# Kernel tuning notes

Hardware: AMD Instinct MI355X
Metric: run time of the kernel (lower is better)

Reference implementation:

```python
import jax, jax.numpy as jnp
import numpy as np

# Genotype (DARTS RNN): 8 recurrent steps (activation, predecessor index) + concat indices
GENO = [("relu", 0), ("relu", 1), ("tanh", 2), ("relu", 3),
        ("relu", 4), ("identity", 1), ("relu", 5), ("relu", 1)]
CONCAT = [1, 2, 3, 4, 5, 6, 7, 8]
NINP, NHID = 256, 256
T, B = 1024, 64
INITRANGE = 0.04

_ACT = {"tanh": jnp.tanh, "relu": jax.nn.relu,
        "sigmoid": jax.nn.sigmoid, "identity": lambda v: v}


def setup_inputs() -> dict:
    key = jax.random.key(0)
    k1, k2, k3, k4 = jax.random.split(key, 4)
    inputs = jax.random.normal(k1, (T, B, NINP), dtype=jnp.float32)
    hidden = jax.random.normal(k2, (1, B, NHID), dtype=jnp.float32)
    W0 = jax.random.uniform(k3, (NINP + NHID, 2 * NHID), dtype=jnp.float32,
                            minval=-INITRANGE, maxval=INITRANGE)
    Ws = jax.random.uniform(k4, (len(GENO), NHID, 2 * NHID), dtype=jnp.float32,
                            minval=-INITRANGE, maxval=INITRANGE)
    return {"inputs": inputs, "hidden": hidden, "W0": W0, "Ws": Ws}


def _cell(x, h_prev, W0, Ws):
    # init state: s0 = h_prev + sigmoid(c0) * (tanh(h0) - h_prev)
    xh = jnp.concatenate([x, h_prev], axis=-1)          # [B, ninp+nhid]
    c0, h0 = jnp.split(xh @ W0, 2, axis=-1)             # each [B, nhid]
    s0 = h_prev + jax.nn.sigmoid(c0) * (jnp.tanh(h0) - h_prev)
    states = [s0]
    for i, (name, pred) in enumerate(GENO):
        s_prev = states[pred]
        c, h = jnp.split(s_prev @ Ws[i], 2, axis=-1)
        states.append(s_prev + jax.nn.sigmoid(c) * (_ACT[name](h) - s_prev))
    return jnp.mean(jnp.stack([states[i] for i in CONCAT], axis=-1), axis=-1)


def reference(inputs, hidden, W0, Ws):
    h0 = hidden[0]  # [B, nhid]

    def step(h, x):
        h_new = _cell(x, h, W0, Ws)
        return h_new, h_new

    _, hiddens = jax.lax.scan(step, h0, inputs)  # [T, B, nhid]
    return hiddens, hiddens[-1][None]
```

## Files before the change

### kernel.cpp

```cpp
#include <hip/hip_runtime.h>


#define TT 1024
#define NWG 16

typedef __attribute__((ext_vector_type(8))) short bf16x8;
typedef __attribute__((ext_vector_type(4))) float f32x4;
typedef __attribute__((ext_vector_type(2))) unsigned int u32x2;

__device__ __forceinline__ unsigned short f2bf(float f) {
  unsigned u = __builtin_bit_cast(unsigned, f);
  u += 0x7FFFu + ((u >> 16) & 1u);
  return (unsigned short)(u >> 16);
}
__device__ __forceinline__ float sigm(float c) { return 1.0f / (1.0f + __expf(-c)); }
__device__ __forceinline__ float tanh_f(float h) {
  float e = __expf(2.0f * h);
  return 1.0f - 2.0f / (e + 1.0f);
}

__device__ __forceinline__ void lda_sc(bf16x8& r, const void* p) {
  asm volatile("global_load_dwordx4 %0, %1, off sc0 sc1" : "=v"(r) : "v"(p));
}
#define ASM_WAIT8(A) asm volatile("s_waitcnt vmcnt(0)" \
  : "+v"((A)[0]), "+v"((A)[1]), "+v"((A)[2]), "+v"((A)[3]), \
    "+v"((A)[4]), "+v"((A)[5]), "+v"((A)[6]), "+v"((A)[7]) :: "memory")

__global__ void darts_init(const float* __restrict__ hid,
                           unsigned short* __restrict__ sf,
                           unsigned* __restrict__ flags) {
  int tid = blockIdx.x * 256 + threadIdx.x;
  if (tid < 512) flags[tid] = 0;
  int lane = tid & 63, mt = (tid >> 6) & 3, kc = tid >> 8;
  const float* ph = hid + (mt * 16 + (lane & 15)) * 256 + kc * 32 + (lane >> 4) * 8;
  bf16x8 v;
#pragma unroll
  for (int e = 0; e < 8; ++e) v[e] = (short)f2bf(ph[e]);
  *(bf16x8*)(sf + 6 * 16384 + tid * 8) = v;
}

__global__ void __launch_bounds__(256, 1) darts_main(
    const float* __restrict__ x, const float* __restrict__ hid,
    const float* __restrict__ W0g, const float* __restrict__ Wsg,
    float* __restrict__ out,
    unsigned short* __restrict__ sf, unsigned* __restrict__ flags) {
  extern __shared__ char sm[];
  const int wg = blockIdx.x, tid = threadIdx.x;
  const int wv = tid >> 6;
  const int lane = tid & 63;

  for (int c = 0; c < 32; ++c) {
    int flat = tid + 256 * c;
    int fl = flat & 63, kc = (flat >> 6) & 7, n = (flat >> 9) & 1, gi = flat >> 10;
    int col = n * 256 + wg * 16 + (fl & 15);
    int kb = kc * 32 + (fl >> 4) * 8;
    bf16x8 v;
#pragma unroll
    for (int e = 0; e < 8; ++e) v[e] = (short)f2bf(Wsg[(gi * 256 + kb + e) * 512 + col]);
    *(bf16x8*)(&sm[flat * 16]) = v;
  }

  bf16x8 w0c[16], w0h[16];
#pragma unroll
  for (int kc = 0; kc < 16; ++kc) {
    int kb = kc * 32 + (lane >> 4) * 8;
    bf16x8 vc, vh;
#pragma unroll
    for (int e = 0; e < 8; ++e) {
      vc[e] = (short)f2bf(W0g[(kb + e) * 512 + wg * 16 + (lane & 15)]);
      vh[e] = (short)f2bf(W0g[(kb + e) * 512 + 256 + wg * 16 + (lane & 15)]);
    }
    w0c[kc] = vc; w0h[kc] = vh;
  }

  const int m = wv * 16 + (lane & 15);
  const int n0 = wg * 16 + (lane >> 4) * 4;

  float hprev[4];
  float st[9][4];
  {
    f32x4 h4 = *(const f32x4*)(hid + m * 256 + n0);
#pragma unroll
    for (int r = 0; r < 4; ++r) hprev[r] = h4[r];
  }

  const int wbase = ((((wg >> 1) * 4 + wv) * 64 +
                      (lane & 15) + 16 * ((wg * 2 + (lane >> 5)) & 3)) * 8) +
                    ((lane >> 4) & 1) * 4;

  __syncthreads();

  unsigned short* sfh = sf + 6 * 16384;
  const unsigned* const pollp = flags + (lane & 15);
  float* const outp = out + (size_t)m * 256 + n0;

#define PUBLISH(TOK) do { \
    unsigned tk_ = (unsigned)(TOK); \
    asm volatile("s_waitcnt vmcnt(0)" ::: "memory"); \
    __syncthreads(); \
    if (tid == 0) \
      asm volatile("global_store_dword %0, %1, off sc0 sc1" \
                   :: "v"(flags + wg), "v"(tk_) : "memory"); \
  } while (0)

#define POLL(TOK) do { \
    unsigned tk_ = (unsigned)(TOK); \
    if (tk_) { \
      if (wv == 0) { \
        unsigned fv_; \
        do { \
          asm volatile("global_load_dword %0, %1, off sc0 sc1\n\t" \
                       "s_waitcnt vmcnt(0)" \
                       : "=v"(fv_) : "v"(pollp) : "memory"); \
        } while (__any((int)(fv_ < tk_))); \
      } \
      __syncthreads(); \
    } \
  } while (0)

#define GBAR(TOK) do { PUBLISH(TOK); POLL(TOK); } while (0)

#define LOADA(BUF) do { _Pragma("unroll") \
    for (int kc = 0; kc < 8; ++kc) \
      lda_sc(a[kc], (const unsigned short*)(BUF) + ((kc * 4 + wv) * 64 + lane) * 8); \
    ASM_WAIT8(a); \
  } while (0)

#define MM(GI, AC, AH) do { _Pragma("unroll") \
    for (int kc = 0; kc < 8; ++kc) { \
      bf16x8 bc = *(const bf16x8*)(&sm[((((GI) * 2 + 0) * 8 + kc) * 64 + lane) * 16]); \
      bf16x8 bh = *(const bf16x8*)(&sm[((((GI) * 2 + 1) * 8 + kc) * 64 + lane) * 16]); \
      AC = __builtin_amdgcn_mfma_f32_16x16x32_bf16(bc, a[kc], AC, 0, 0, 0); \
      AH = __builtin_amdgcn_mfma_f32_16x16x32_bf16(bh, a[kc], AH, 0, 0, 0); \
    } } while (0)

#define UPD(SI, PR, ACT, AC, AH) do { _Pragma("unroll") \
    for (int r = 0; r < 4; ++r) { \
      float g = sigm((AC)[r]); float hh = (AH)[r]; \
      float av = (ACT) == 0 ? fmaxf(hh, 0.0f) : ((ACT) == 1 ? tanh_f(hh) : hh); \
      st[SI][r] = st[PR][r] + g * (av - st[PR][r]); \
    } } while (0)

#define STOREF(BUF, SI) do { \
    unsigned lo_ = (unsigned)f2bf(st[SI][0]) | ((unsigned)f2bf(st[SI][1]) << 16); \
    unsigned hi_ = (unsigned)f2bf(st[SI][2]) | ((unsigned)f2bf(st[SI][3]) << 16); \
    u32x2 v_; v_[0] = lo_; v_[1] = hi_; \
    asm volatile("global_store_dwordx2 %0, %1, off sc0 sc1" \
                 :: "v"((unsigned short*)(BUF) + wbase), "v"(v_) : "memory"); \
  } while (0)

#pragma clang loop unroll(disable)
  for (int t = 0; t < TT; ++t) {
    f32x4 c0 = {0, 0, 0, 0}, h0 = {0, 0, 0, 0};
    {
      bf16x8 ax[8];
#pragma unroll
      for (int kc = 0; kc < 8; ++kc) {
        const float* px = x + ((t * 64 + m) * 256 + kc * 32 + (lane >> 4) * 8);
        bf16x8 v;
#pragma unroll
        for (int e = 0; e < 8; ++e) v[e] = (short)f2bf(px[e]);
        ax[kc] = v;
      }
#pragma unroll
      for (int kc = 0; kc < 8; ++kc) {
        c0 = __builtin_amdgcn_mfma_f32_16x16x32_bf16(w0c[kc], ax[kc], c0, 0, 0, 0);
        h0 = __builtin_amdgcn_mfma_f32_16x16x32_bf16(w0h[kc], ax[kc], h0, 0, 0, 0);
      }
    }
    POLL(t * 7);
    {
      bf16x8 ahf[8];
#pragma unroll
      for (int kc = 0; kc < 8; ++kc)
        lda_sc(ahf[kc], sfh + ((kc * 4 + wv) * 64 + lane) * 8);
      ASM_WAIT8(ahf);
#pragma unroll
      for (int kc = 0; kc < 8; ++kc) {
        c0 = __builtin_amdgcn_mfma_f32_16x16x32_bf16(w0c[8 + kc], ahf[kc], c0, 0, 0, 0);
        h0 = __builtin_amdgcn_mfma_f32_16x16x32_bf16(w0h[8 + kc], ahf[kc], h0, 0, 0, 0);
      }
#pragma unroll
      for (int r = 0; r < 4; ++r) {
        float g = sigm(c0[r]);
        float th = tanh_f(h0[r]);
        st[0][r] = hprev[r] + g * (th - hprev[r]);
      }
      STOREF(sf + 0 * 16384, 0);
    }
    GBAR(t * 7 + 1);

    bf16x8 a[8];
    {
      LOADA(sf + 0 * 16384);
      f32x4 ac = {0, 0, 0, 0}, ah = {0, 0, 0, 0};
      MM(0, ac, ah);
      UPD(1, 0, 0, ac, ah);
      STOREF(sf + 1 * 16384, 1);
    }
    GBAR(t * 7 + 2);
    {
      LOADA(sf + 1 * 16384);
      f32x4 c2 = {0, 0, 0, 0}, h2 = {0, 0, 0, 0};
      MM(1, c2, h2);
      UPD(2, 1, 0, c2, h2);
      STOREF(sf + 2 * 16384, 2);
      PUBLISH(t * 7 + 3);
      f32x4 c6 = {0, 0, 0, 0}, h6 = {0, 0, 0, 0}, c8 = {0, 0, 0, 0}, h8 = {0, 0, 0, 0};
      MM(5, c6, h6); MM(7, c8, h8);
      UPD(6, 1, 2, c6, h6);
      UPD(8, 1, 0, c8, h8);
      POLL(t * 7 + 3);
    }
    {
      LOADA(sf + 2 * 16384);
      f32x4 ac = {0, 0, 0, 0}, ah = {0, 0, 0, 0};
      MM(2, ac, ah);
      UPD(3, 2, 1, ac, ah);
      STOREF(sf + 3 * 16384, 3);
    }
    GBAR(t * 7 + 4);
    {
      LOADA(sf + 3 * 16384);
      f32x4 ac = {0, 0, 0, 0}, ah = {0, 0, 0, 0};
      MM(3, ac, ah);
      UPD(4, 3, 0, ac, ah);
      STOREF(sf + 4 * 16384, 4);
    }
    GBAR(t * 7 + 5);
    {
      LOADA(sf + 4 * 16384);
      f32x4 ac = {0, 0, 0, 0}, ah = {0, 0, 0, 0};
      MM(4, ac, ah);
      UPD(5, 4, 0, ac, ah);
      STOREF(sf + 5 * 16384, 5);
    }
    GBAR(t * 7 + 6);
    {
      LOADA(sf + 5 * 16384);
      f32x4 ac = {0, 0, 0, 0}, ah = {0, 0, 0, 0};
      MM(6, ac, ah);
      UPD(7, 5, 0, ac, ah);
      float hv[4];
#pragma unroll
      for (int r = 0; r < 4; ++r) {
        hv[r] = (st[1][r] + st[2][r] + st[3][r] + st[4][r] +
                 st[5][r] + st[6][r] + st[7][r] + st[8][r]) * 0.125f;
        hprev[r] = hv[r];
      }
      {
        unsigned lo_ = (unsigned)f2bf(hv[0]) | ((unsigned)f2bf(hv[1]) << 16);
        unsigned hi_ = (unsigned)f2bf(hv[2]) | ((unsigned)f2bf(hv[3]) << 16);
        u32x2 v_; v_[0] = lo_; v_[1] = hi_;
        asm volatile("global_store_dwordx2 %0, %1, off sc0 sc1"
                     :: "v"(sfh + wbase), "v"(v_) : "memory");
      }
      PUBLISH(t * 7 + 7);
      f32x4 o4 = {hv[0], hv[1], hv[2], hv[3]};
      *(f32x4*)(outp + (size_t)t * 16384) = o4;
      if (t == TT - 1) *(f32x4*)(out + 16777216 + (size_t)m * 256 + n0) = o4;
    }
  }
#undef PUBLISH
#undef POLL
#undef GBAR
#undef LOADA
#undef MM
#undef UPD
#undef STOREF
}

extern "C" void kernel_launch(void* const* d_in, const int* in_sizes, int n_in,
                              void* d_out, int out_size, void* d_ws, size_t ws_size,
                              hipStream_t stream) {
  const float* x   = (const float*)d_in[0];
  const float* hid = (const float*)d_in[1];
  const float* W0  = (const float*)d_in[2];
  const float* Ws  = (const float*)d_in[3];
  float* out = (float*)d_out;
  unsigned short* sf = (unsigned short*)d_ws;
  unsigned* flags = (unsigned*)((char*)d_ws + 7 * 32768);

  hipFuncSetAttribute((const void*)darts_main,
                      hipFuncAttributeMaxDynamicSharedMemorySize, 131072);
  darts_init<<<8, 256, 0, stream>>>(hid, sf, flags);
  darts_main<<<NWG, 256, 131072, stream>>>(x, hid, W0, Ws, out, sf, flags);
}
```

Before: 19.86 ms.

## Co-locate all workgroups on one XCC and sync through L2 instead of MALL

The kernel now launches 256 workgroups. Each one reads its XCC id and joins an atomic election, and only the first 16 workgroups on the first XCC to fill up stay; the rest exit. Because every worker then shares one L2, state loads and stores drop the sc1 (system/MALL) coherence bit. Flags are published to both an L2 copy and a MALL copy, and polling checks L2 first, falling back to MALL after 16 tries. The aim is to cut the cross-workgroup barrier latency that dominates the 7 syncs per timestep. The cost is the election overhead, and correctness now depends on all 16 workgroups actually sharing an L2.

```diff
diff --git a/kernel.cpp b/kernel.cpp
--- a/kernel.cpp
+++ b/kernel.cpp
@@ -20,7 +20,7 @@
 }
 
 __device__ __forceinline__ void lda_sc(bf16x8& r, const void* p) {
-  asm volatile("global_load_dwordx4 %0, %1, off sc0 sc1" : "=v"(r) : "v"(p));
+  asm volatile("global_load_dwordx4 %0, %1, off sc0" : "=v"(r) : "v"(p));
 }
 #define ASM_WAIT8(A) asm volatile("s_waitcnt vmcnt(0)" \
   : "+v"((A)[0]), "+v"((A)[1]), "+v"((A)[2]), "+v"((A)[3]), \
@@ -44,8 +44,32 @@
     const float* __restrict__ W0g, const float* __restrict__ Wsg,
     float* __restrict__ out,
     unsigned short* __restrict__ sf, unsigned* __restrict__ flags) {
+  const int tid = threadIdx.x;
+  unsigned xcc = __builtin_amdgcn_s_getreg(6164) & 0xFu;
+  __shared__ unsigned s_slot;
+  if (tid == 0) {
+    unsigned res = 0xFFFFFFFFu;
+    unsigned slot = __hip_atomic_fetch_add(&flags[64 + xcc * 16], 1u,
+                                           __ATOMIC_RELAXED, __HIP_MEMORY_SCOPE_AGENT);
+    if (slot < NWG) {
+      if (slot == NWG - 1) {
+        unsigned exp = 0u;
+        __hip_atomic_compare_exchange_strong(&flags[320], &exp, xcc + 1u,
+            __ATOMIC_RELAXED, __ATOMIC_RELAXED, __HIP_MEMORY_SCOPE_AGENT);
+      }
+      unsigned c;
+      do {
+        c = __hip_atomic_load(&flags[320], __ATOMIC_RELAXED, __HIP_MEMORY_SCOPE_AGENT);
+      } while (c == 0u);
+      if (c == xcc + 1u) res = slot;
+    }
+    s_slot = res;
+  }
+  __syncthreads();
+  if (s_slot >= NWG) return;
+  const int wg = (int)s_slot;
+
   extern __shared__ char sm[];
-  const int wg = blockIdx.x, tid = threadIdx.x;
   const int wv = tid >> 6;
   const int lane = tid & 63;
 
@@ -91,28 +115,39 @@
   __syncthreads();
 
   unsigned short* sfh = sf + 6 * 16384;
-  const unsigned* const pollp = flags + (lane & 15);
+  const unsigned* const pollMALL = flags + (lane & 15);
+  const unsigned* const pollL2 = flags + 16 + (lane & 15);
   float* const outp = out + (size_t)m * 256 + n0;
 
 #define PUBLISH(TOK) do { \
     unsigned tk_ = (unsigned)(TOK); \
     asm volatile("s_waitcnt vmcnt(0)" ::: "memory"); \
     __syncthreads(); \
-    if (tid == 0) \
+    if (tid == 0) { \
+      asm volatile("global_store_dword %0, %1, off sc0" \
+                   :: "v"(flags + 16 + wg), "v"(tk_) : "memory"); \
       asm volatile("global_store_dword %0, %1, off sc0 sc1" \
                    :: "v"(flags + wg), "v"(tk_) : "memory"); \
+    } \
   } while (0)
 
 #define POLL(TOK) do { \
     unsigned tk_ = (unsigned)(TOK); \
     if (tk_) { \
       if (wv == 0) { \
-        unsigned fv_; \
-        do { \
-          asm volatile("global_load_dword %0, %1, off sc0 sc1\n\t" \
+        unsigned fv_; int it_ = 0; \
+        for (;;) { \
+          asm volatile("global_load_dword %0, %1, off sc0\n\t" \
                        "s_waitcnt vmcnt(0)" \
-                       : "=v"(fv_) : "v"(pollp) : "memory"); \
-        } while (__any((int)(fv_ < tk_))); \
+                       : "=v"(fv_) : "v"(pollL2) : "memory"); \
+          if (!__any((int)(fv_ < tk_))) break; \
+          if (++it_ >= 16) { \
+            asm volatile("global_load_dword %0, %1, off sc0 sc1\n\t" \
+                         "s_waitcnt vmcnt(0)" \
+                         : "=v"(fv_) : "v"(pollMALL) : "memory"); \
+            if (!__any((int)(fv_ < tk_))) break; \
+          } \
+        } \
       } \
       __syncthreads(); \
     } \
@@ -145,7 +180,7 @@
     unsigned lo_ = (unsigned)f2bf(st[SI][0]) | ((unsigned)f2bf(st[SI][1]) << 16); \
     unsigned hi_ = (unsigned)f2bf(st[SI][2]) | ((unsigned)f2bf(st[SI][3]) << 16); \
     u32x2 v_; v_[0] = lo_; v_[1] = hi_; \
-    asm volatile("global_store_dwordx2 %0, %1, off sc0 sc1" \
+    asm volatile("global_store_dwordx2 %0, %1, off sc0" \
                  :: "v"((unsigned short*)(BUF) + wbase), "v"(v_) : "memory"); \
   } while (0)
 
@@ -252,7 +287,7 @@
         unsigned lo_ = (unsigned)f2bf(hv[0]) | ((unsigned)f2bf(hv[1]) << 16);
         unsigned hi_ = (unsigned)f2bf(hv[2]) | ((unsigned)f2bf(hv[3]) << 16);
         u32x2 v_; v_[0] = lo_; v_[1] = hi_;
-        asm volatile("global_store_dwordx2 %0, %1, off sc0 sc1"
+        asm volatile("global_store_dwordx2 %0, %1, off sc0"
                      :: "v"(sfh + wbase), "v"(v_) : "memory");
       }
       PUBLISH(t * 7 + 7);
@@ -284,5 +319,5 @@
   hipFuncSetAttribute((const void*)darts_main,
                       hipFuncAttributeMaxDynamicSharedMemorySize, 131072);
   darts_init<<<8, 256, 0, stream>>>(hid, sf, flags);
-  darts_main<<<NWG, 256, 131072, stream>>>(x, hid, W0, Ws, out, sf, flags);
-}
+  darts_main<<<256, 256, 131072, stream>>>(x, hid, W0, Ws, out, sf, flags);
+}
```

After: 30.60 ms. 54.1% more time.
